# Optimization experiments

Hardware: AMD Instinct MI355X
Metric: run time of the kernel (lower is better)

## Reference

```python
import jax, jax.numpy as jnp
import numpy as np

N_NODES = 100000
N_EDGES = 1600000
IN_C, HID_C, OUT_C = 128, 128, 64


def setup_inputs() -> dict:
    key = jax.random.key(0)
    ks = jax.random.split(key, 8)
    x = jax.random.normal(ks[0], (N_NODES, IN_C), dtype=jnp.float32)
    edge_index = jax.random.randint(ks[1], (2, N_EDGES), 0, N_NODES, dtype=jnp.int32)
    # Glorot-ish init for GCNConv linear weights, zero bias (PyG default)
    def glorot(k, fan_in, fan_out):
        s = jnp.sqrt(6.0 / (fan_in + fan_out))
        return jax.random.uniform(k, (fan_in, fan_out), dtype=jnp.float32, minval=-s, maxval=s)
    return {
        "x": x,
        "edge_index": edge_index,
        "W1": glorot(ks[2], IN_C, HID_C), "b1": jnp.zeros((HID_C,), jnp.float32),
        "W2": glorot(ks[3], HID_C, HID_C), "b2": jnp.zeros((HID_C,), jnp.float32),
        "W3": glorot(ks[4], HID_C, OUT_C), "b3": jnp.zeros((OUT_C,), jnp.float32),
    }


def _gcn_norm(edge_index, num_nodes):
    # Add self-loops (PyG GCNConv default) and compute symmetric normalization
    loops = jnp.arange(num_nodes, dtype=edge_index.dtype)
    src = jnp.concatenate([edge_index[0], loops])  # [E+N]
    dst = jnp.concatenate([edge_index[1], loops])
    deg = jax.ops.segment_sum(jnp.ones_like(dst, dtype=jnp.float32), dst,
                              num_segments=num_nodes)
    deg_inv_sqrt = jnp.where(deg > 0, jax.lax.rsqrt(jnp.maximum(deg, 1.0)), 0.0)
    norm = deg_inv_sqrt[src] * deg_inv_sqrt[dst]  # [E+N]
    return src, dst, norm


def _gcn_layer(x, src, dst, norm, W, b, num_nodes):
    h = x @ W                                # [N, out] dense transform first
    msg = h[src] * norm[:, None]             # gather + scale  [E+N, out]
    out = jax.ops.segment_sum(msg, dst, num_segments=num_nodes)  # scatter-add
    return out + b


def reference(x, edge_index, W1, b1, W2, b2, W3, b3):
    n = x.shape[0]
    src, dst, norm = _gcn_norm(edge_index, n)
    h = jax.nn.relu(_gcn_layer(x, src, dst, norm, W1, b1, n))
    h = jax.nn.relu(_gcn_layer(h, src, dst, norm, W2, b2, n))
    return _gcn_layer(h, src, dst, norm, W3, b3, n)
```

## Files before the change

kernel.cpp:

```cpp
#include <hip/hip_runtime.h>

#define NN 100000
#define NE 1600000
#define NBK 98
#define BSH 10
#define MPAD 100096
#define SCB 391
#define CAP 20480

typedef unsigned short ushortT;
typedef unsigned long long ull;
using sh8 = __attribute__((ext_vector_type(8))) short;
using f4  = __attribute__((ext_vector_type(4))) float;


__device__ __forceinline__ unsigned short bfr(float f) {
  unsigned u = __float_as_uint(f);
  u += 0x7FFF + ((u >> 16) & 1);
  return (unsigned short)(u >> 16);
}
__device__ __forceinline__ float bf2f(unsigned short h) {
  return __uint_as_float(((unsigned)h) << 16);
}
__device__ __forceinline__ void split2(float a, float b, unsigned& H, unsigned& L) {
  unsigned short ha = bfr(a), hb = bfr(b);
  H = (unsigned)ha | ((unsigned)hb << 16);
  L = (unsigned)bfr(a - bf2f(ha)) | ((unsigned)bfr(b - bf2f(hb)) << 16);
}
__device__ __forceinline__ void acc8(const uint4 v, float* a) {
  a[0] += __uint_as_float(v.x << 16);
  a[1] += __uint_as_float(v.x & 0xFFFF0000u);
  a[2] += __uint_as_float(v.y << 16);
  a[3] += __uint_as_float(v.y & 0xFFFF0000u);
  a[4] += __uint_as_float(v.z << 16);
  a[5] += __uint_as_float(v.z & 0xFFFF0000u);
  a[6] += __uint_as_float(v.w << 16);
  a[7] += __uint_as_float(v.w & 0xFFFF0000u);
}
__device__ __forceinline__ sh8 hi8(const float4 a, const float4 b) {
  sh8 r;
  r[0] = (short)bfr(a.x); r[1] = (short)bfr(a.y);
  r[2] = (short)bfr(a.z); r[3] = (short)bfr(a.w);
  r[4] = (short)bfr(b.x); r[5] = (short)bfr(b.y);
  r[6] = (short)bfr(b.z); r[7] = (short)bfr(b.w);
  return r;
}
__device__ __forceinline__ sh8 lo8(const float4 a, const float4 b, const sh8 h) {
  sh8 r;
  r[0] = (short)bfr(a.x - bf2f((unsigned short)h[0]));
  r[1] = (short)bfr(a.y - bf2f((unsigned short)h[1]));
  r[2] = (short)bfr(a.z - bf2f((unsigned short)h[2]));
  r[3] = (short)bfr(a.w - bf2f((unsigned short)h[3]));
  r[4] = (short)bfr(b.x - bf2f((unsigned short)h[4]));
  r[5] = (short)bfr(b.y - bf2f((unsigned short)h[5]));
  r[6] = (short)bfr(b.z - bf2f((unsigned short)h[6]));
  r[7] = (short)bfr(b.w - bf2f((unsigned short)h[7]));
  return r;
}


template <int COUT>
__device__ __forceinline__ void packone(const float* __restrict__ W,
                                        ushortT* __restrict__ Bp, int i) {
  const int j = i & 7;
  const int l = (i >> 3) & 63;
  const int rest = i >> 9;
  const int g = rest % (COUT / 16);
  const int ks = rest / (COUT / 16);
  const int k = (ks & 3) * 32 + (l >> 4) * 8 + j;
  const int n = g * 16 + (l & 15);
  const float v = W[k * COUT + n];
  const unsigned short h = bfr(v);
  Bp[i] = (ks < 4) ? h : bfr(v - bf2f(h));
}


__global__ __launch_bounds__(256) void k_scatterpack(
    const int* __restrict__ src, const int* __restrict__ dst,
    int* __restrict__ cursor, ull* __restrict__ pairArr,
    const float* __restrict__ W1, const float* __restrict__ W2,
    const float* __restrict__ W3, ushortT* __restrict__ Bp1,
    ushortT* __restrict__ Bp2, ushortT* __restrict__ Bp3) {
  if (blockIdx.x >= SCB) {
    const int i = (blockIdx.x - SCB) * 256 + threadIdx.x;
    if (i < 32768) packone<128>(W1, Bp1, i);
    else if (i < 65536) packone<128>(W2, Bp2, i - 32768);
    else packone<64>(W3, Bp3, i - 65536);
    return;
  }
  __shared__ int lcnt[NBK];
  __shared__ int lbase[NBK];
  __shared__ int lrank[NBK];
  __shared__ int bbase[NBK];
  __shared__ ull sorted[4096];
  __shared__ int target[4096];
  const int t = threadIdx.x;
  for (int i = t; i < NBK; i += 256) { lcnt[i] = 0; lrank[i] = 0; }
  __syncthreads();
  const int base = blockIdx.x * 4096;
  int rs[16], rd[16];
#pragma unroll
  for (int q = 0; q < 16; q++) {
    int e = base + t + 256 * q;
    rs[q] = (e < NE) ? src[e] : -1;
    rd[q] = (e < NE) ? dst[e] : -1;
    if (rd[q] >= 0) atomicAdd(&lcnt[rd[q] >> BSH], 1);
  }
  __syncthreads();
  if (t == 0) {
    int run = 0;
    for (int i = 0; i < NBK; i++) { lbase[i] = run; run += lcnt[i]; }
  }
  __syncthreads();
  if (t < NBK && lcnt[t] > 0) bbase[t] = atomicAdd(&cursor[t], lcnt[t]);
  __syncthreads();
#pragma unroll
  for (int q = 0; q < 16; q++) {
    if (rd[q] >= 0) {
      int b = rd[q] >> BSH;
      int r = atomicAdd(&lrank[b], 1);
      int slot = lbase[b] + r;
      sorted[slot] = ((ull)(unsigned)rs[q] << 32) | (unsigned)rd[q];
      target[slot] = b * CAP + bbase[b] + r;
    }
  }
  __syncthreads();
  const int n = min(4096, NE - base);
  for (int s = t; s < n; s += 256) pairArr[target[s]] = sorted[s];
}


__global__ __launch_bounds__(256) void k_buildcsr(const ull* __restrict__ pairArr,
                                                  const int* __restrict__ cnt,
                                                  float* __restrict__ dinv,
                                                  int* __restrict__ rowptr,
                                                  int* __restrict__ col) {
  __shared__ int lc[1024];
  __shared__ int sd[256];
  __shared__ int bc[NBK];
  __shared__ int ebegS;
  const int t = threadIdx.x;
  const int b = blockIdx.x;
  const int n0 = b << BSH;
  if (t < NBK) bc[t] = cnt[t];
  for (int i = t; i < 1024; i += 256) lc[i] = 0;
  __syncthreads();
  if (t == 0) {
    int run = 0;
    for (int i = 0; i < b; i++) run += bc[i];
    ebegS = run;
  }
  __syncthreads();
  const int ebeg = ebegS;
  const int myCnt = bc[b];
  const ull* pb = pairArr + (size_t)b * CAP;
  for (int i = t; i < myCnt; i += 256)
    atomicAdd(&lc[(int)(unsigned)(pb[i] & 0xffffffffULL) - n0], 1);
  __syncthreads();
  const int v0 = lc[t * 4], v1 = lc[t * 4 + 1], v2 = lc[t * 4 + 2], v3 = lc[t * 4 + 3];
  const int s = v0 + v1 + v2 + v3;
  sd[t] = s;
  __syncthreads();
  for (int off = 1; off < 256; off <<= 1) {
    int x = (t >= off) ? sd[t - off] : 0;
    __syncthreads();
    sd[t] += x;
    __syncthreads();
  }
  const int run = sd[t] - s;
  const int c0 = run, c1 = run + v0, c2 = c1 + v1, c3 = c2 + v2;
  lc[t * 4] = c0; lc[t * 4 + 1] = c1; lc[t * 4 + 2] = c2; lc[t * 4 + 3] = c3;
  const int cnts[4] = {v0, v1, v2, v3};
  const int curs[4] = {c0, c1, c2, c3};
#pragma unroll
  for (int i = 0; i < 4; i++) {
    int node = n0 + t * 4 + i;
    if (node < NN) {
      rowptr[node] = ebeg + curs[i];
      dinv[node] = rsqrtf(1.0f + (float)cnts[i]);
    }
  }
  if (b == 0 && t == 0) rowptr[NN] = NE;
  __syncthreads();
  for (int i = t; i < myCnt; i += 256) {
    ull p = pb[i];
    int d = (int)(unsigned)(p & 0xffffffffULL);
    int srcv = (int)(unsigned)(p >> 32);
    int pos = atomicAdd(&lc[d - n0], 1);
    col[ebeg + pos] = srcv;
  }
}


template <int COUT, bool FUSED>
__global__ __launch_bounds__(256) void k_gemmM(const ushortT* __restrict__ A2,
                                               const float* __restrict__ X,
                                               const ushortT* __restrict__ Bp,
                                               const float* __restrict__ dinv,
                                               ushortT* __restrict__ hs) {
  constexpr int CGALL = COUT / 16;
  constexpr int RG = 2;
  constexpr int CG = 4;
  const int w = threadIdx.x >> 6;
  const int lane = threadIdx.x & 63;
  const int q = lane >> 4;
  const int c = lane & 15;
  int row0, cg0;
  if (COUT == 128) {
    row0 = blockIdx.x * 64 + (w & 1) * 32;
    cg0 = (w >> 1) * 4;
  } else {
    row0 = blockIdx.x * 128 + w * 32;
    cg0 = 0;
  }

  const ushortT* ap[RG];
  const float* xp[RG];
#pragma unroll
  for (int rg = 0; rg < RG; rg++) {
    const int row = row0 + rg * 16 + c;
    if (FUSED) xp[rg] = X + (size_t)min(row, NN - 1) * 128 + q * 8;
    else ap[rg] = A2 + (size_t)row * 256 + q * 8;
  }
  const ushortT* bp0 = Bp + (size_t)lane * 8;

  f4 acc[RG][CG];
#pragma unroll
  for (int i = 0; i < RG; i++)
#pragma unroll
    for (int j = 0; j < CG; j++) acc[i][j] = (f4){0.f, 0.f, 0.f, 0.f};

  sh8 ah[RG], al[RG], bh[CG], bl[CG];
  sh8 nah[RG], nal[RG], nbh[CG], nbl[CG];

  auto loadA = [&](int kr, sh8 (&h)[RG], sh8 (&l)[RG]) {
#pragma unroll
    for (int rg = 0; rg < RG; rg++) {
      if (FUSED) {
        const float4 x0 = *reinterpret_cast<const float4*>(xp[rg] + kr * 32);
        const float4 x1 = *reinterpret_cast<const float4*>(xp[rg] + kr * 32 + 4);
        h[rg] = hi8(x0, x1);
        l[rg] = lo8(x0, x1, h[rg]);
      } else {
        h[rg] = *reinterpret_cast<const sh8*>(ap[rg] + kr * 32);
        l[rg] = *reinterpret_cast<const sh8*>(ap[rg] + 128 + kr * 32);
      }
    }
  };
  auto loadB = [&](int kr, sh8 (&h)[CG], sh8 (&l)[CG]) {
#pragma unroll
    for (int cg = 0; cg < CG; cg++) {
      h[cg] = *reinterpret_cast<const sh8*>(bp0 + (size_t)(kr * CGALL + cg0 + cg) * 512);
      l[cg] = *reinterpret_cast<const sh8*>(bp0 + (size_t)((4 + kr) * CGALL + cg0 + cg) * 512);
    }
  };

  loadA(0, ah, al);
  loadB(0, bh, bl);
#pragma unroll
  for (int kr = 0; kr < 4; kr++) {
    if (kr < 3) {
      loadA(kr + 1, nah, nal);
      loadB(kr + 1, nbh, nbl);
    }
#pragma unroll
    for (int rg = 0; rg < RG; rg++)
#pragma unroll
      for (int cg = 0; cg < CG; cg++)
        acc[rg][cg] = __builtin_amdgcn_mfma_f32_16x16x32_bf16(ah[rg], bh[cg],
                                                              acc[rg][cg], 0, 0, 0);
#pragma unroll
    for (int rg = 0; rg < RG; rg++)
#pragma unroll
      for (int cg = 0; cg < CG; cg++)
        acc[rg][cg] = __builtin_amdgcn_mfma_f32_16x16x32_bf16(al[rg], bh[cg],
                                                              acc[rg][cg], 0, 0, 0);
#pragma unroll
    for (int rg = 0; rg < RG; rg++)
#pragma unroll
      for (int cg = 0; cg < CG; cg++)
        acc[rg][cg] = __builtin_amdgcn_mfma_f32_16x16x32_bf16(ah[rg], bl[cg],
                                                              acc[rg][cg], 0, 0, 0);
    if (kr < 3) {
#pragma unroll
      for (int rg = 0; rg < RG; rg++) { ah[rg] = nah[rg]; al[rg] = nal[rg]; }
#pragma unroll
      for (int cg = 0; cg < CG; cg++) { bh[cg] = nbh[cg]; bl[cg] = nbl[cg]; }
    }
  }

#pragma unroll
  for (int rg = 0; rg < RG; rg++) {
#pragma unroll
    for (int reg = 0; reg < 4; reg++) {
      const int row = row0 + rg * 16 + q * 4 + reg;
      if (row < NN) {
        const float dv = dinv[row];
#pragma unroll
        for (int cg = 0; cg < CG; cg++) {
          hs[(size_t)row * COUT + (cg0 + cg) * 16 + c] = bfr(acc[rg][cg][reg] * dv);
        }
      }
    }
  }
}


template <bool RELU>
__global__ __launch_bounds__(256) void k_agg128(const ushortT* __restrict__ hs,
                                                const int* __restrict__ rowptr,
                                                const int* __restrict__ col,
                                                const float* __restrict__ dinv,
                                                const float* __restrict__ bias,
                                                ushortT* __restrict__ A2) {
  const int gid = blockIdx.x * 256 + threadIdx.x;
  const int node = gid >> 6;
  if (node >= NN) return;
  const int lane = threadIdx.x & 63;
  const int q = lane >> 4;
  const int chb = (lane & 15) * 8;
  const int beg = rowptr[node];
  const int end = rowptr[node + 1];

  float a[8] = {};
  if (q == 0) {
    const uint4 v = *reinterpret_cast<const uint4*>(hs + (long)node * 128 + chb);
    acc8(v, a);
  }

  int j = beg;
  if (j + 8 <= end) {
    int c0 = col[j + q];
    int c1 = col[j + 4 + q];
    while (true) {
      const uint4 v0 = *reinterpret_cast<const uint4*>(hs + (long)c0 * 128 + chb);
      const uint4 v1 = *reinterpret_cast<const uint4*>(hs + (long)c1 * 128 + chb);
      j += 8;
      const bool more = (j + 8 <= end);
      int n0, n1;
      if (more) { n0 = col[j + q]; n1 = col[j + 4 + q]; }
      acc8(v0, a);
      acc8(v1, a);
      if (!more) break;
      c0 = n0; c1 = n1;
    }
  }
  for (; j + 4 <= end; j += 4) {
    int c = col[j + q];
    const uint4 v = *reinterpret_cast<const uint4*>(hs + (long)c * 128 + chb);
    acc8(v, a);
  }
  {
    const int r = end - j;
    if (q < r) {
      int c = col[j + q];
      const uint4 v = *reinterpret_cast<const uint4*>(hs + (long)c * 128 + chb);
      acc8(v, a);
    }
  }

#pragma unroll
  for (int i = 0; i < 8; i++) a[i] += __shfl(a[i], lane ^ 32);
#pragma unroll
  for (int i = 0; i < 8; i++) a[i] += __shfl(a[i], lane ^ 16);

  if (q == 0) {
    const float di = dinv[node];
    const float4 b0 = *reinterpret_cast<const float4*>(bias + chb);
    const float4 b1 = *reinterpret_cast<const float4*>(bias + chb + 4);
    float o[8];
    o[0] = fmaf(a[0], di, b0.x); o[1] = fmaf(a[1], di, b0.y);
    o[2] = fmaf(a[2], di, b0.z); o[3] = fmaf(a[3], di, b0.w);
    o[4] = fmaf(a[4], di, b1.x); o[5] = fmaf(a[5], di, b1.y);
    o[6] = fmaf(a[6], di, b1.z); o[7] = fmaf(a[7], di, b1.w);
    if (RELU) {
#pragma unroll
      for (int i = 0; i < 8; i++) o[i] = fmaxf(o[i], 0.f);
    }
    uint4 H, L;
    split2(o[0], o[1], H.x, L.x);
    split2(o[2], o[3], H.y, L.y);
    split2(o[4], o[5], H.z, L.z);
    split2(o[6], o[7], H.w, L.w);
    *reinterpret_cast<uint4*>(A2 + (long)node * 256 + chb) = H;
    *reinterpret_cast<uint4*>(A2 + (long)node * 256 + 128 + chb) = L;
  }
}

__global__ __launch_bounds__(256) void k_agg64(const ushortT* __restrict__ hs,
                                               const int* __restrict__ rowptr,
                                               const int* __restrict__ col,
                                               const float* __restrict__ dinv,
                                               const float* __restrict__ bias,
                                               float* __restrict__ out) {
  const int gid = blockIdx.x * 256 + threadIdx.x;
  const int node = gid >> 6;
  if (node >= NN) return;
  const int lane = threadIdx.x & 63;
  const int o8 = lane >> 3;
  const int chb = (lane & 7) * 8;
  const int beg = rowptr[node];
  const int end = rowptr[node + 1];

  float a[8] = {};
  if (o8 == 0) {
    const uint4 v = *reinterpret_cast<const uint4*>(hs + (long)node * 64 + chb);
    acc8(v, a);
  }

  int j = beg;
  if (j + 16 <= end) {
    int c0 = col[j + o8];
    int c1 = col[j + 8 + o8];
    while (true) {
      const uint4 v0 = *reinterpret_cast<const uint4*>(hs + (long)c0 * 64 + chb);
      const uint4 v1 = *reinterpret_cast<const uint4*>(hs + (long)c1 * 64 + chb);
      j += 16;
      const bool more = (j + 16 <= end);
      int n0, n1;
      if (more) { n0 = col[j + o8]; n1 = col[j + 8 + o8]; }
      acc8(v0, a);
      acc8(v1, a);
      if (!more) break;
      c0 = n0; c1 = n1;
    }
  }
  for (; j + 8 <= end; j += 8) {
    int c = col[j + o8];
    const uint4 v = *reinterpret_cast<const uint4*>(hs + (long)c * 64 + chb);
    acc8(v, a);
  }
  {
    const int r = end - j;
    if (o8 < r) {
      int c = col[j + o8];
      const uint4 v = *reinterpret_cast<const uint4*>(hs + (long)c * 64 + chb);
      acc8(v, a);
    }
  }

#pragma unroll
  for (int i = 0; i < 8; i++) a[i] += __shfl(a[i], lane ^ 32);
#pragma unroll
  for (int i = 0; i < 8; i++) a[i] += __shfl(a[i], lane ^ 16);
#pragma unroll
  for (int i = 0; i < 8; i++) a[i] += __shfl(a[i], lane ^ 8);

  if (o8 == 0) {
    const float di = dinv[node];
    const float4 b0 = *reinterpret_cast<const float4*>(bias + chb);
    const float4 b1 = *reinterpret_cast<const float4*>(bias + chb + 4);
    float4 r0, r1;
    r0.x = fmaf(a[0], di, b0.x); r0.y = fmaf(a[1], di, b0.y);
    r0.z = fmaf(a[2], di, b0.z); r0.w = fmaf(a[3], di, b0.w);
    r1.x = fmaf(a[4], di, b1.x); r1.y = fmaf(a[5], di, b1.y);
    r1.z = fmaf(a[6], di, b1.z); r1.w = fmaf(a[7], di, b1.w);
    *reinterpret_cast<float4*>(out + (long)node * 64 + chb) = r0;
    *reinterpret_cast<float4*>(out + (long)node * 64 + chb + 4) = r1;
  }
}


extern "C" void kernel_launch(void* const* d_in, const int* in_sizes, int n_in,
                              void* d_out, int out_size, void* d_ws, size_t ws_size,
                              hipStream_t stream) {
  const float* x  = (const float*)d_in[0];
  const int* ei   = (const int*)d_in[1];
  const float* W1 = (const float*)d_in[2];
  const float* b1 = (const float*)d_in[3];
  const float* W2 = (const float*)d_in[4];
  const float* b2 = (const float*)d_in[5];
  const float* W3 = (const float*)d_in[6];
  const float* b3 = (const float*)d_in[7];
  float* out = (float*)d_out;
  const int* srcp = ei;
  const int* dstp = ei + NE;

  char* wsb = (char*)d_ws;
  size_t off = 0;
  auto alloc = [&](size_t bytes) -> void* {
    void* p = wsb + off;
    off += (bytes + 255) & ~(size_t)255;
    return p;
  };
  ushortT* A2  = (ushortT*)alloc((size_t)MPAD * 256 * 2);
  ushortT* hs  = (ushortT*)alloc((size_t)NN * 128 * 2);
  int*   col    = (int*)alloc((size_t)NE * 4);
  int*   rowptr = (int*)alloc((size_t)(NN + 1) * 4);
  float* dinv   = (float*)alloc((size_t)NN * 4);
  int*   cursor = (int*)alloc((size_t)NBK * 4);
  ushortT* Bp1 = (ushortT*)alloc((size_t)32768 * 2);
  ushortT* Bp2 = (ushortT*)alloc((size_t)32768 * 2);
  ushortT* Bp3 = (ushortT*)alloc((size_t)16384 * 2);
  ull* pairArr = (ull*)hs;
  (void)ws_size; (void)in_sizes; (void)n_in; (void)out_size;

  hipMemsetAsync(cursor, 0, (size_t)NBK * 4, stream);
  k_scatterpack<<<SCB + 320, 256, 0, stream>>>(srcp, dstp, cursor, pairArr,
                                               W1, W2, W3, Bp1, Bp2, Bp3);
  k_buildcsr<<<NBK, 256, 0, stream>>>(pairArr, cursor, dinv, rowptr, col);

  const int aggGrid = (NN * 64) / 256;
  const int gemmGrid128 = MPAD / 64;
  const int gemmGrid64 = MPAD / 128;

  k_gemmM<128, true><<<gemmGrid128, 256, 0, stream>>>(nullptr, x, Bp1, dinv, hs);
  k_agg128<true><<<aggGrid, 256, 0, stream>>>(hs, rowptr, col, dinv, b1, A2);
  k_gemmM<128, false><<<gemmGrid128, 256, 0, stream>>>(A2, nullptr, Bp2, dinv, hs);
  k_agg128<true><<<aggGrid, 256, 0, stream>>>(hs, rowptr, col, dinv, b2, A2);
  k_gemmM<64, false><<<gemmGrid64, 256, 0, stream>>>(A2, nullptr, Bp3, dinv, hs);
  k_agg64<<<aggGrid, 256, 0, stream>>>(hs, rowptr, col, dinv, b3, out);
}
```

Before: 409.2 us.

## Drop low-half bf16 split of activations and widen CSR build blocks

Activations are now stored and fed to the MFMA GEMMs as a single bf16 value instead of a hi/lo bf16 pair. This halves the A-matrix traffic and removes one third of the MFMAs; the weight hi/lo split is kept. The CSR build kernel now runs with 1024 threads per block, one node per thread, and uses a longer scan. The cost is lower accuracy, since activations carry only bf16 precision.

```diff
diff --git a/kernel.cpp b/kernel.cpp
--- a/kernel.cpp
+++ b/kernel.cpp
@@ -21,11 +21,6 @@
 }
 __device__ __forceinline__ float bf2f(unsigned short h) {
   return __uint_as_float(((unsigned)h) << 16);
-}
-__device__ __forceinline__ void split2(float a, float b, unsigned& H, unsigned& L) {
-  unsigned short ha = bfr(a), hb = bfr(b);
-  H = (unsigned)ha | ((unsigned)hb << 16);
-  L = (unsigned)bfr(a - bf2f(ha)) | ((unsigned)bfr(b - bf2f(hb)) << 16);
 }
 __device__ __forceinline__ void acc8(const uint4 v, float* a) {
   a[0] += __uint_as_float(v.x << 16);
@@ -43,18 +38,6 @@
   r[2] = (short)bfr(a.z); r[3] = (short)bfr(a.w);
   r[4] = (short)bfr(b.x); r[5] = (short)bfr(b.y);
   r[6] = (short)bfr(b.z); r[7] = (short)bfr(b.w);
-  return r;
-}
-__device__ __forceinline__ sh8 lo8(const float4 a, const float4 b, const sh8 h) {
-  sh8 r;
-  r[0] = (short)bfr(a.x - bf2f((unsigned short)h[0]));
-  r[1] = (short)bfr(a.y - bf2f((unsigned short)h[1]));
-  r[2] = (short)bfr(a.z - bf2f((unsigned short)h[2]));
-  r[3] = (short)bfr(a.w - bf2f((unsigned short)h[3]));
-  r[4] = (short)bfr(b.x - bf2f((unsigned short)h[4]));
-  r[5] = (short)bfr(b.y - bf2f((unsigned short)h[5]));
-  r[6] = (short)bfr(b.z - bf2f((unsigned short)h[6]));
-  r[7] = (short)bfr(b.w - bf2f((unsigned short)h[7]));
   return r;
 }
 
@@ -130,20 +113,20 @@
 }
 
 
-__global__ __launch_bounds__(256) void k_buildcsr(const ull* __restrict__ pairArr,
-                                                  const int* __restrict__ cnt,
-                                                  float* __restrict__ dinv,
-                                                  int* __restrict__ rowptr,
-                                                  int* __restrict__ col) {
+__global__ __launch_bounds__(1024) void k_buildcsr(const ull* __restrict__ pairArr,
+                                                   const int* __restrict__ cnt,
+                                                   float* __restrict__ dinv,
+                                                   int* __restrict__ rowptr,
+                                                   int* __restrict__ col) {
   __shared__ int lc[1024];
-  __shared__ int sd[256];
+  __shared__ int sd[1024];
   __shared__ int bc[NBK];
   __shared__ int ebegS;
   const int t = threadIdx.x;
   const int b = blockIdx.x;
   const int n0 = b << BSH;
   if (t < NBK) bc[t] = cnt[t];
-  for (int i = t; i < 1024; i += 256) lc[i] = 0;
+  lc[t] = 0;
   __syncthreads();
   if (t == 0) {
     int run = 0;
@@ -154,35 +137,28 @@
   const int ebeg = ebegS;
   const int myCnt = bc[b];
   const ull* pb = pairArr + (size_t)b * CAP;
-  for (int i = t; i < myCnt; i += 256)
+  for (int i = t; i < myCnt; i += 1024)
     atomicAdd(&lc[(int)(unsigned)(pb[i] & 0xffffffffULL) - n0], 1);
   __syncthreads();
-  const int v0 = lc[t * 4], v1 = lc[t * 4 + 1], v2 = lc[t * 4 + 2], v3 = lc[t * 4 + 3];
-  const int s = v0 + v1 + v2 + v3;
-  sd[t] = s;
-  __syncthreads();
-  for (int off = 1; off < 256; off <<= 1) {
+  const int v = lc[t];
+  sd[t] = v;
+  __syncthreads();
+  for (int off = 1; off < 1024; off <<= 1) {
     int x = (t >= off) ? sd[t - off] : 0;
     __syncthreads();
     sd[t] += x;
     __syncthreads();
   }
-  const int run = sd[t] - s;
-  const int c0 = run, c1 = run + v0, c2 = c1 + v1, c3 = c2 + v2;
-  lc[t * 4] = c0; lc[t * 4 + 1] = c1; lc[t * 4 + 2] = c2; lc[t * 4 + 3] = c3;
-  const int cnts[4] = {v0, v1, v2, v3};
-  const int curs[4] = {c0, c1, c2, c3};
-#pragma unroll
-  for (int i = 0; i < 4; i++) {
-    int node = n0 + t * 4 + i;
-    if (node < NN) {
-      rowptr[node] = ebeg + curs[i];
-      dinv[node] = rsqrtf(1.0f + (float)cnts[i]);
-    }
+  const int excl = sd[t] - v;
+  lc[t] = excl;
+  const int node = n0 + t;
+  if (node < NN) {
+    rowptr[node] = ebeg + excl;
+    dinv[node] = rsqrtf(1.0f + (float)v);
   }
   if (b == 0 && t == 0) rowptr[NN] = NE;
   __syncthreads();
-  for (int i = t; i < myCnt; i += 256) {
+  for (int i = t; i < myCnt; i += 1024) {
     ull p = pb[i];
     int d = (int)(unsigned)(p & 0xffffffffULL);
     int srcv = (int)(unsigned)(p >> 32);
@@ -193,7 +169,7 @@
 
 
 template <int COUT, bool FUSED>
-__global__ __launch_bounds__(256) void k_gemmM(const ushortT* __restrict__ A2,
+__global__ __launch_bounds__(256) void k_gemmM(const ushortT* __restrict__ A,
                                                const float* __restrict__ X,
                                                const ushortT* __restrict__ Bp,
                                                const float* __restrict__ dinv,
@@ -220,7 +196,7 @@
   for (int rg = 0; rg < RG; rg++) {
     const int row = row0 + rg * 16 + c;
     if (FUSED) xp[rg] = X + (size_t)min(row, NN - 1) * 128 + q * 8;
-    else ap[rg] = A2 + (size_t)row * 256 + q * 8;
+    else ap[rg] = A + (size_t)row * 128 + q * 8;
   }
   const ushortT* bp0 = Bp + (size_t)lane * 8;
 
@@ -230,20 +206,18 @@
 #pragma unroll
     for (int j = 0; j < CG; j++) acc[i][j] = (f4){0.f, 0.f, 0.f, 0.f};
 
-  sh8 ah[RG], al[RG], bh[CG], bl[CG];
-  sh8 nah[RG], nal[RG], nbh[CG], nbl[CG];
-
-  auto loadA = [&](int kr, sh8 (&h)[RG], sh8 (&l)[RG]) {
+  sh8 ah[RG], bh[CG], bl[CG];
+  sh8 nah[RG], nbh[CG], nbl[CG];
+
+  auto loadA = [&](int kr, sh8 (&h)[RG]) {
 #pragma unroll
     for (int rg = 0; rg < RG; rg++) {
       if (FUSED) {
         const float4 x0 = *reinterpret_cast<const float4*>(xp[rg] + kr * 32);
         const float4 x1 = *reinterpret_cast<const float4*>(xp[rg] + kr * 32 + 4);
         h[rg] = hi8(x0, x1);
-        l[rg] = lo8(x0, x1, h[rg]);
       } else {
         h[rg] = *reinterpret_cast<const sh8*>(ap[rg] + kr * 32);
-        l[rg] = *reinterpret_cast<const sh8*>(ap[rg] + 128 + kr * 32);
       }
     }
   };
@@ -255,12 +229,12 @@
     }
   };
 
-  loadA(0, ah, al);
+  loadA(0, ah);
   loadB(0, bh, bl);
 #pragma unroll
   for (int kr = 0; kr < 4; kr++) {
     if (kr < 3) {
-      loadA(kr + 1, nah, nal);
+      loadA(kr + 1, nah);
       loadB(kr + 1, nbh, nbl);
     }
 #pragma unroll
@@ -268,12 +242,6 @@
 #pragma unroll
       for (int cg = 0; cg < CG; cg++)
         acc[rg][cg] = __builtin_amdgcn_mfma_f32_16x16x32_bf16(ah[rg], bh[cg],
-                                                              acc[rg][cg], 0, 0, 0);
-#pragma unroll
-    for (int rg = 0; rg < RG; rg++)
-#pragma unroll
-      for (int cg = 0; cg < CG; cg++)
-        acc[rg][cg] = __builtin_amdgcn_mfma_f32_16x16x32_bf16(al[rg], bh[cg],
                                                               acc[rg][cg], 0, 0, 0);
 #pragma unroll
     for (int rg = 0; rg < RG; rg++)
@@ -283,7 +251,7 @@
                                                               acc[rg][cg], 0, 0, 0);
     if (kr < 3) {
 #pragma unroll
-      for (int rg = 0; rg < RG; rg++) { ah[rg] = nah[rg]; al[rg] = nal[rg]; }
+      for (int rg = 0; rg < RG; rg++) ah[rg] = nah[rg];
 #pragma unroll
       for (int cg = 0; cg < CG; cg++) { bh[cg] = nbh[cg]; bl[cg] = nbl[cg]; }
     }
@@ -312,7 +280,7 @@
                                                 const int* __restrict__ col,
                                                 const float* __restrict__ dinv,
                                                 const float* __restrict__ bias,
-                                                ushortT* __restrict__ A2) {
+                                                ushortT* __restrict__ A) {
   const int gid = blockIdx.x * 256 + threadIdx.x;
   const int node = gid >> 6;
   if (node >= NN) return;
@@ -377,13 +345,12 @@
 #pragma unroll
       for (int i = 0; i < 8; i++) o[i] = fmaxf(o[i], 0.f);
     }
-    uint4 H, L;
-    split2(o[0], o[1], H.x, L.x);
-    split2(o[2], o[3], H.y, L.y);
-    split2(o[4], o[5], H.z, L.z);
-    split2(o[6], o[7], H.w, L.w);
-    *reinterpret_cast<uint4*>(A2 + (long)node * 256 + chb) = H;
-    *reinterpret_cast<uint4*>(A2 + (long)node * 256 + 128 + chb) = L;
+    uint4 H;
+    H.x = (unsigned)bfr(o[0]) | ((unsigned)bfr(o[1]) << 16);
+    H.y = (unsigned)bfr(o[2]) | ((unsigned)bfr(o[3]) << 16);
+    H.z = (unsigned)bfr(o[4]) | ((unsigned)bfr(o[5]) << 16);
+    H.w = (unsigned)bfr(o[6]) | ((unsigned)bfr(o[7]) << 16);
+    *reinterpret_cast<uint4*>(A + (long)node * 128 + chb) = H;
   }
 }
 
@@ -483,7 +450,7 @@
     off += (bytes + 255) & ~(size_t)255;
     return p;
   };
-  ushortT* A2  = (ushortT*)alloc((size_t)MPAD * 256 * 2);
+  ushortT* A   = (ushortT*)alloc((size_t)MPAD * 128 * 2);
   ushortT* hs  = (ushortT*)alloc((size_t)NN * 128 * 2);
   int*   col    = (int*)alloc((size_t)NE * 4);
   int*   rowptr = (int*)alloc((size_t)(NN + 1) * 4);
@@ -498,16 +465,16 @@
   hipMemsetAsync(cursor, 0, (size_t)NBK * 4, stream);
   k_scatterpack<<<SCB + 320, 256, 0, stream>>>(srcp, dstp, cursor, pairArr,
                                                W1, W2, W3, Bp1, Bp2, Bp3);
-  k_buildcsr<<<NBK, 256, 0, stream>>>(pairArr, cursor, dinv, rowptr, col);
+  k_buildcsr<<<NBK, 1024, 0, stream>>>(pairArr, cursor, dinv, rowptr, col);
 
   const int aggGrid = (NN * 64) / 256;
   const int gemmGrid128 = MPAD / 64;
   const int gemmGrid64 = MPAD / 128;
 
   k_gemmM<128, true><<<gemmGrid128, 256, 0, stream>>>(nullptr, x, Bp1, dinv, hs);
-  k_agg128<true><<<aggGrid, 256, 0, stream>>>(hs, rowptr, col, dinv, b1, A2);
-  k_gemmM<128, false><<<gemmGrid128, 256, 0, stream>>>(A2, nullptr, Bp2, dinv, hs);
-  k_agg128<true><<<aggGrid, 256, 0, stream>>>(hs, rowptr, col, dinv, b2, A2);
-  k_gemmM<64, false><<<gemmGrid64, 256, 0, stream>>>(A2, nullptr, Bp3, dinv, hs);
+  k_agg128<true><<<aggGrid, 256, 0, stream>>>(hs, rowptr, col, dinv, b1, A);
+  k_gemmM<128, false><<<gemmGrid128, 256, 0, stream>>>(A, nullptr, Bp2, dinv, hs);
+  k_agg128<true><<<aggGrid, 256, 0, stream>>>(hs, rowptr, col, dinv, b2, A);
+  k_gemmM<64, false><<<gemmGrid64, 256, 0, stream>>>(A, nullptr, Bp3, dinv, hs);
   k_agg64<<<aggGrid, 256, 0, stream>>>(hs, rowptr, col, dinv, b3, out);
 }
```

Result: faster. 372.1 us (-9.1%).
